# Optimization experiments

Measured on AMD Instinct MI355X. Metric: run time of the kernel, lower is better.

The kernel has to match this reference:

```python
import jax, jax.numpy as jnp
import numpy as np

EMB_DIM = 512
QKV_DIM = 512
NUM_HEADS = 8
HEAD_DIM = QKV_DIM // NUM_HEADS  # 64
BATCH = 4
SEQLEN = 2048


def _gaussian_orthogonal_random_matrix(rng, nb_rows, nb_cols):
    # Matches torch gaussian_orthogonal_random_matrix with scaling=0.
    blocks = []
    n_full = nb_rows // nb_cols
    for _ in range(n_full):
        q, _ = np.linalg.qr(rng.standard_normal((nb_cols, nb_cols)))
        blocks.append(q.T)
    rem = nb_rows - n_full * nb_cols
    if rem > 0:
        q, _ = np.linalg.qr(rng.standard_normal((nb_cols, nb_cols)))
        blocks.append(q.T[:rem])
    mat = np.concatenate(blocks, axis=0)
    mult = np.linalg.norm(rng.standard_normal((nb_rows, nb_cols)), axis=1)
    return (mult[:, None] * mat).astype(np.float32)


def setup_inputs() -> dict:
    key = jax.random.key(0)
    ks = jax.random.split(key, 9)
    s = 0.02
    inp = {
        'x': jax.random.normal(ks[0], (BATCH, SEQLEN, EMB_DIM), jnp.float32),
        'Wq': jax.random.normal(ks[1], (EMB_DIM, QKV_DIM), jnp.float32) * s,
        'bq': jnp.zeros((QKV_DIM,), jnp.float32),
        'Wk': jax.random.normal(ks[2], (EMB_DIM, QKV_DIM), jnp.float32) * s,
        'bk': jnp.zeros((QKV_DIM,), jnp.float32),
        'Wv': jax.random.normal(ks[3], (EMB_DIM, QKV_DIM), jnp.float32) * s,
        'bv': jnp.zeros((QKV_DIM,), jnp.float32),
        'Wo': jax.random.normal(ks[4], (QKV_DIM, EMB_DIM), jnp.float32) * s,
        'bo': jnp.zeros((EMB_DIM,), jnp.float32),
        'proj': jnp.asarray(_gaussian_orthogonal_random_matrix(
            np.random.default_rng(0), QKV_DIM, HEAD_DIM)),  # (m=qkv_dim, head_dim)
    }
    return inp


def _split_heads(x):
    b, s, _ = x.shape
    return x.reshape(b, s, NUM_HEADS, HEAD_DIM).transpose(0, 2, 1, 3)  # (b,h,s,d)


def _softmax_kernel(data, proj, is_query, eps=1e-4):
    # data: (b,h,n,d); proj: (m,d)
    d = data.shape[-1]
    dn = d ** -0.25                       # data normalizer
    ratio = proj.shape[0] ** -0.5         # m^{-1/2}
    data_dash = jnp.einsum('bhnd,md->bhnm', dn * data, proj)
    diag = jnp.sum(data * data, axis=-1, keepdims=True) * (0.5 * dn * dn)
    if is_query:
        m = jax.lax.stop_gradient(jnp.max(data_dash, axis=-1, keepdims=True))
    else:
        m = jax.lax.stop_gradient(jnp.max(data_dash, axis=(-1, -2), keepdims=True))
    return ratio * (jnp.exp(data_dash - diag - m) + eps)


def _linear_attn(q, k, v):
    # q,k: (b,h,n,m); v: (b,h,n,d)
    k_cumsum = jnp.sum(k, axis=-2)                                  # (b,h,m)
    d_inv = 1.0 / jnp.einsum('bhnm,bhm->bhn', q, k_cumsum)          # (b,h,n)
    context = jnp.einsum('bhnm,bhnd->bhmd', k, v)                   # (b,h,m,d)
    return jnp.einsum('bhmd,bhnm,bhn->bhnd', context, q, d_inv)


def reference(x, Wq, bq, Wk, bk, Wv, bv, Wo, bo, proj):
    q = _split_heads(x @ Wq + bq)
    k = _split_heads(x @ Wk + bk)
    v = _split_heads(x @ Wv + bv)
    qp = _softmax_kernel(q, proj, is_query=True)
    kp = _softmax_kernel(k, proj, is_query=False)
    out = _linear_attn(qp, kp, v)                                   # (b,h,n,d)
    b, h, n, d = out.shape
    out = out.transpose(0, 2, 1, 3).reshape(b, n, h * d)            # combine heads
    return out @ Wo + bo
```

## Files before the change

kernel.cpp:

```cpp
#include <hip/hip_runtime.h>

typedef unsigned short u16;
typedef unsigned int   u32;
typedef __attribute__((ext_vector_type(8))) short bf16x8;
typedef __attribute__((ext_vector_type(4))) short s16x4;
typedef __attribute__((ext_vector_type(4))) float f32x4;

#define MFMA16(a,b,c) __builtin_amdgcn_mfma_f32_16x16x32_bf16((a),(b),(c),0,0,0)

__device__ __forceinline__ float bf2f(u16 u){ return __uint_as_float(((u32)u)<<16); }
__device__ __forceinline__ u16 f2bf(float f){
  u32 u = __float_as_uint(f);
  return (u16)((u + 0x7fffu + ((u>>16)&1u)) >> 16);
}
__device__ __forceinline__ u32 encf(float f){ u32 u=__float_as_uint(f); return (u&0x80000000u)? ~u : (u|0x80000000u); }
__device__ __forceinline__ float decf(u32 u){ return (u&0x80000000u)? __uint_as_float(u&0x7fffffffu) : __uint_as_float(~u); }

__device__ __forceinline__ void async_lds16(u16* lds, const u16* g){
  __builtin_amdgcn_global_load_lds((const __attribute__((address_space(1))) void*)g,
                                   (__attribute__((address_space(3))) void*)lds,
                                   16, 0, 0);
}

template<int ROWS>
__device__ __forceinline__ void stage64(u16* dst, const u16* src, int srcStride, int tid){
  #pragma unroll
  for (int u=tid; u<ROWS*8; u+=256){
    int r=u>>3, c=(u&7)<<3;
    *(int4*)&dst[r*72+c] = *(const int4*)&src[(size_t)r*srcStride + c];
  }
}

__global__ void k_init(u32* kmaxEnc, u16* projS,
                       const float* __restrict__ proj, const float* __restrict__ x, u16* __restrict__ xb){
  int i = blockIdx.x*blockDim.x + threadIdx.x;
  int st = gridDim.x*blockDim.x;
  for (int j=i; j<32; j+=st) kmaxEnc[j]=0u;
  const float dn = 0.35355339059327373f;
  for (int j=i; j<512*64; j+=st) projS[j] = f2bf(dn*proj[j]);
  for (int j=i; j<524288; j+=st){
    float4 a = *(const float4*)&x[(size_t)j*8];
    float4 b = *(const float4*)&x[(size_t)j*8+4];
    u16 tmp[8] = {f2bf(a.x),f2bf(a.y),f2bf(a.z),f2bf(a.w),
                  f2bf(b.x),f2bf(b.y),f2bf(b.z),f2bf(b.w)};
    *(int4*)&xb[(size_t)j*8] = *(const int4*)tmp;
  }
}

__global__ __launch_bounds__(256) void k_trw(const float* s0, const float* s1, const float* s2, const float* s3,
                                             u16* d0, u16* d1, u16* d2, u16* d3){
  int z = blockIdx.z;
  const float* src = z==0?s0:(z==1?s1:(z==2?s2:s3));
  u16* dst         = z==0?d0:(z==1?d1:(z==2?d2:d3));
  __shared__ u16 t[32][34];
  int c0=blockIdx.x*32, r0=blockIdx.y*32;
  int tid=threadIdx.x;
  for (int u=tid; u<1024; u+=256){ int r=u>>5, c=u&31; t[r][c]=f2bf(src[(size_t)(r0+r)*512 + c0+c]); }
  __syncthreads();
  for (int u=tid; u<1024; u+=256){ int c=u>>5, r=u&31; dst[(size_t)(c0+c)*512 + r0+r]=t[r][c]; }
}

__global__ __launch_bounds__(256) void k_trv(const u16* __restrict__ v, u16* __restrict__ vT){
  int bh = blockIdx.z; int b=bh>>3, h=bh&7;
  int d0 = blockIdx.x*32, n0 = blockIdx.y*32;
  __shared__ u16 t[32][34];
  int tid=threadIdx.x;
  const u16* s = v + (size_t)(b*2048)*512 + h*64;
  for (int u=tid; u<1024; u+=256){ int r=u>>5, c=u&31; t[r][c]=s[(size_t)(n0+r)*512 + d0+c]; }
  __syncthreads();
  u16* d = vT + (size_t)bh*64*2048;
  for (int u=tid; u<1024; u+=256){ int c=u>>5, r=u&31; d[(size_t)(d0+c)*2048 + n0+r]=t[r][c]; }
}

__global__ __launch_bounds__(256) void k_vsum(const u16* __restrict__ vB, float* __restrict__ vsum){
  int bh=blockIdx.x; int b=bh>>3, h=bh&7;
  int tid=threadIdx.x; int d=tid&63, part=tid>>6;
  const u16* src = vB + (size_t)(b*2048 + part*512)*512 + h*64 + d;
  float s=0.f;
  for (int n=0;n<512;++n) s += bf2f(src[(size_t)n*512]);
  __shared__ float red[256];
  red[tid]=s; __syncthreads();
  if (part==0) vsum[bh*64+d]=red[d]+red[64+d]+red[128+d]+red[192+d];
}

__global__ __launch_bounds__(256) void k_kdiag(const u16* __restrict__ kB, float* __restrict__ diagK){
  int bh=blockIdx.x, seg=blockIdx.y;
  int b=bh>>3, h=bh&7;
  int tid=threadIdx.x;
  int part=tid&7;
  const u16* base = kB + (size_t)(b*2048 + seg*256)*512 + h*64 + part*8;
  for (int n0=0; n0<256; n0+=32){
    int n = n0 + (tid>>3);
    bf16x8 v = *(const bf16x8*)&base[(size_t)n*512];
    float sq=0.f;
    #pragma unroll
    for (int j=0;j<8;++j){ float f=bf2f((u16)v[j]); sq+=f*f; }
    sq += __shfl_xor(sq,1,64); sq += __shfl_xor(sq,2,64); sq += __shfl_xor(sq,4,64);
    if (part==0) diagK[(size_t)bh*2048 + seg*256 + n] = 0.0625f*sq;
  }
}

__global__ __launch_bounds__(256) void k_sums(const u16* __restrict__ ctxT, const float* __restrict__ kcs,
                                              float* __restrict__ ctxsum, float* __restrict__ kcssum){
  int bh = blockIdx.x;
  int tid = threadIdx.x;
  int d = tid&63, part = tid>>6;
  const u16* src = ctxT + (size_t)bh*64*512 + (size_t)d*512 + part*128;
  float s=0.f;
  for (int m=0;m<128;m+=8){
    bf16x8 v = *(const bf16x8*)&src[m];
    #pragma unroll
    for (int j=0;j<8;++j) s += bf2f((u16)v[j]);
  }
  __shared__ float red[256];
  __shared__ float red2[256];
  red[tid]=s;
  float t=0.f;
  for (int u=tid;u<512;u+=256) t += kcs[(size_t)bh*512+u];
  red2[tid]=t;
  __syncthreads();
  if (part==0) ctxsum[bh*64+d] = red[d]+red[64+d]+red[128+d]+red[192+d];
  if (tid<64){
    float a=red2[tid]+red2[tid+64]+red2[tid+128]+red2[tid+192];
    #pragma unroll
    for (int m2=1;m2<64;m2<<=1) a += __shfl_xor(a,m2,64);
    if (tid==0) kcssum[bh]=a;
  }
}

template<bool OF32>
__global__ __launch_bounds__(256) void k_gemm2(const u16* __restrict__ A,
    const u16* BT0, const u16* BT1, const u16* BT2,
    const float* b0, const float* b1, const float* b2,
    void* O0, void* O1, void* O2)
{
  int z = blockIdx.z;
  const u16* BT    = z==0?BT0:(z==1?BT1:BT2);
  const float* bias= z==0?b0 :(z==1?b1 :b2 );
  void* Ov         = z==0?O0 :(z==1?O1 :O2 );
  int bm = blockIdx.x*128, bn = blockIdx.y*64;
  __shared__ u16 sA[128*64];
  __shared__ u16 sB[64*64];
  int tid=threadIdx.x, w=tid>>6, lane=tid&63;
  int lr = lane>>3, lc = (lane&7)*8;
  f32x4 acc[8] = {};
  for (int kk=0; kk<512; kk+=64){
    __syncthreads();
    #pragma unroll
    for (int i=0;i<4;++i){
      int idx = w*4+i;
      async_lds16(&sA[idx*512], A + (size_t)(bm + idx*8 + lr)*512 + kk + lc);
    }
    #pragma unroll
    for (int i=0;i<2;++i){
      int idx = w*2+i;
      async_lds16(&sB[idx*512], BT + (size_t)(bn + idx*8 + lr)*512 + kk + lc);
    }
    __syncthreads();
    int fr = lane&15, kb=(lane>>4)*8;
    #pragma unroll
    for (int rt=0; rt<2; ++rt){
      int ar = (w*2+rt)*16 + fr;
      #pragma unroll
      for (int ct=0; ct<4; ++ct){
        int br = ct*16 + fr;
        #pragma unroll
        for (int kc=0; kc<2; ++kc){
          bf16x8 av = *(const bf16x8*)&sA[ar*64 + kc*32 + kb];
          bf16x8 bv = *(const bf16x8*)&sB[br*64 + kc*32 + kb];
          acc[rt*4+ct] = MFMA16(av,bv,acc[rt*4+ct]);
        }
      }
    }
  }
  int colg = lane&15, rowg=(lane>>4)*4;
  #pragma unroll
  for (int rt=0; rt<2; ++rt){
    #pragma unroll
    for (int ct=0; ct<4; ++ct){
      int col = bn + ct*16 + colg;
      float bv = bias[col];
      #pragma unroll
      for (int j=0;j<4;++j){
        int row = bm + (w*2+rt)*16 + rowg + j;
        if constexpr (OF32) ((float*)Ov)[(size_t)row*512 + col] = acc[rt*4+ct][j] + bv;
        else                ((u16*) Ov)[(size_t)row*512 + col] = f2bf(acc[rt*4+ct][j] + bv);
      }
    }
  }
}

__global__ __launch_bounds__(256) void k_kpctx3(const u16* __restrict__ kB, const u16* __restrict__ projS,
    const u16* __restrict__ vT, const float* __restrict__ diagK,
    float* __restrict__ ctxPT, float* __restrict__ kcsP, u32* __restrict__ kmaxEnc)
{
  int h=blockIdx.x, y=blockIdx.y, b=blockIdx.z;
  int mblk = y&7, s = y>>3;
  int bh=b*8+h;
  int m0 = mblk*64;
  __shared__ __align__(16) u16 sK[128*72];
  __shared__ __align__(16) u16 sV[64*136];
  __shared__ __align__(16) u16 sP[64*72];
  __shared__ __align__(16) u16 sT[64*136];
  __shared__ float sDg[128];
  __shared__ float red[4];
  int tid=threadIdx.x, w=tid>>6, lane=tid&63;
  int fr=lane&15, kb=(lane>>4)*8, rowg=(lane>>4)*4;
  stage64<64>(sP, projS + m0*64, 64, tid);
  f32x4 accc[4]={};
  float sS=0.f;
  float lm=-3.0e38f;
  const u16* gK = kB + (size_t)(b*2048 + s*1024)*512 + h*64;
  const u16* gV = vT + (size_t)bh*64*2048 + s*1024;
  const float* gD = diagK + (size_t)bh*2048 + s*1024;
  int4 pK[4], pV[4]; float4 pD={0.f,0.f,0.f,0.f};
  #pragma unroll
  for (int i=0;i<4;++i){ int u=tid+i*256; int r=u>>3,c=(u&7)<<3; pK[i]=*(const int4*)&gK[(size_t)r*512 + c]; }
  #pragma unroll
  for (int i=0;i<4;++i){ int u=tid+i*256; int r=u>>4,c=(u&15)<<3; pV[i]=*(const int4*)&gV[(size_t)r*2048 + c]; }
  if (tid<32) pD = *(const float4*)&gD[tid*4];
  for (int nc=0; nc<8; ++nc){
    #pragma unroll
    for (int i=0;i<4;++i){ int u=tid+i*256; int r=u>>3,c=(u&7)<<3; *(int4*)&sK[r*72+c]=pK[i]; }
    #pragma unroll
    for (int i=0;i<4;++i){ int u=tid+i*256; int r=u>>4,c=(u&15)<<3; *(int4*)&sV[r*136+c]=pV[i]; }
    if (tid<32) *(float4*)&sDg[tid*4] = pD;
    __syncthreads();
    if (nc<7){
      #pragma unroll
      for (int i=0;i<4;++i){ int u=tid+i*256; int r=u>>3,c=(u&7)<<3; pK[i]=*(const int4*)&gK[(size_t)((nc+1)*128+r)*512 + c]; }
      #pragma unroll
      for (int i=0;i<4;++i){ int u=tid+i*256; int r=u>>4,c=(u&15)<<3; pV[i]=*(const int4*)&gV[(size_t)r*2048 + (nc+1)*128 + c]; }
      if (tid<32) pD = *(const float4*)&gD[(nc+1)*128 + tid*4];
    }
    f32x4 facc[2][4];
    #pragma unroll
    for (int rt=0;rt<2;++rt){
      int ar=(w*2+rt)*16+fr;
      #pragma unroll
      for (int mt=0;mt<4;++mt){
        f32x4 a={0.f,0.f,0.f,0.f};
        a=MFMA16(*(const bf16x8*)&sK[ar*72+kb],    *(const bf16x8*)&sP[(mt*16+fr)*72+kb],    a);
        a=MFMA16(*(const bf16x8*)&sK[ar*72+32+kb], *(const bf16x8*)&sP[(mt*16+fr)*72+32+kb], a);
        facc[rt][mt]=a;
        lm=fmaxf(lm, fmaxf(fmaxf(a[0],a[1]),fmaxf(a[2],a[3])));
      }
    }
    #pragma unroll
    for (int rt=0;rt<2;++rt){
      int nl=(w*2+rt)*16+rowg;
      #pragma unroll
      for (int mt=0;mt<4;++mt){
        int ml=mt*16+fr;
        s16x4 pk;
        #pragma unroll
        for (int j=0;j<4;++j) pk[j]=(short)f2bf(__expf(facc[rt][mt][j]-sDg[nl+j]));
        *(s16x4*)&sT[ml*136+nl]=pk;
      }
    }
    __syncthreads();
    int am=w*16+fr;
    #pragma unroll
    for (int ct=0;ct<4;++ct){
      #pragma unroll
      for (int ks=0;ks<4;++ks){
        accc[ct]=MFMA16(*(const bf16x8*)&sT[am*136+ks*32+kb],
                        *(const bf16x8*)&sV[(ct*16+fr)*136+ks*32+kb], accc[ct]);
      }
    }
    {
      int m=tid>>2, q=tid&3;
      #pragma unroll
      for (int n8=0;n8<4;++n8){
        bf16x8 v=*(const bf16x8*)&sT[m*136+q*32+n8*8];
        #pragma unroll
        for (int j=0;j<8;++j) sS += bf2f((u16)v[j]);
      }
    }
    __syncthreads();
  }
  {
    int m=tid>>2, q=tid&3;
    float t=sS;
    t += __shfl_xor(t,1,64); t += __shfl_xor(t,2,64);
    if (q==0) kcsP[(size_t)(s*32+bh)*512 + m0 + m] = t;
  }
  #pragma unroll
  for (int m2=1;m2<64;m2<<=1) lm=fmaxf(lm,__shfl_xor(lm,m2,64));
  if (lane==0) red[w]=lm;
  __syncthreads();
  if (tid==0) atomicMax(&kmaxEnc[bh], encf(fmaxf(fmaxf(red[0],red[1]),fmaxf(red[2],red[3]))));
  float* sTf = (float*)sT;
  int mloc = w*16+rowg;
  #pragma unroll
  for (int ct=0;ct<4;++ct){
    #pragma unroll
    for (int j=0;j<4;++j) sTf[(ct*16+fr)*68 + mloc + j] = accc[ct][j];
  }
  __syncthreads();
  for (int u=tid; u<1024; u+=256){
    int r=u>>4, c=(u&15)*4;
    *(float4*)&ctxPT[((size_t)(s*32+bh)*64 + r)*512 + m0 + c] = *(const float4*)&sTf[r*68+c];
  }
}

__global__ __launch_bounds__(256) void k_comb(const float* __restrict__ ctxPT, u16* __restrict__ ctxT,
                                              const float* __restrict__ kcsP, float* __restrict__ kcs){
  int bh=blockIdx.x, dblk=blockIdx.y;
  int tid=threadIdx.x;
  int d0=dblk*8;
  const float* p0 = ctxPT + ((size_t)bh*64 + d0)*512;
  const float* p1 = ctxPT + ((size_t)(32+bh)*64 + d0)*512;
  u16* o = ctxT + ((size_t)bh*64 + d0)*512;
  for (int u=tid; u<1024; u+=256){
    int r=u>>7, c=(u&127)*4;
    float4 a=*(const float4*)&p0[(size_t)r*512+c];
    float4 bq=*(const float4*)&p1[(size_t)r*512+c];
    u16 t[4]={f2bf(a.x+bq.x),f2bf(a.y+bq.y),f2bf(a.z+bq.z),f2bf(a.w+bq.w)};
    *(int2*)&o[(size_t)r*512+c] = *(const int2*)t;
  }
  if (dblk==0){
    for (int u=tid; u<512; u+=256)
      kcs[(size_t)bh*512+u] = kcsP[(size_t)bh*512+u] + kcsP[(size_t)(32+bh)*512+u];
  }
}

__global__ __launch_bounds__(256) void k_qpout2(const u16* __restrict__ qB, const u16* __restrict__ projS,
    const float* __restrict__ kcs, const u16* __restrict__ ctxT,
    const float* __restrict__ ctxsum, const float* __restrict__ kcssum,
    const float* __restrict__ vsum, const u32* __restrict__ kmaxEnc,
    u16* __restrict__ outc)
{
  int h=blockIdx.x, chunk=blockIdx.y, b=blockIdx.z;
  int bh=b*8+h;
  int t0 = b*2048 + chunk*128;
  __shared__ u16 sP[2][64*64];
  __shared__ u16 sCt[2][64*64];
  __shared__ u16 qpL[128*72];
  __shared__ float sK[512];
  __shared__ float diag[128];
  int tid=threadIdx.x, w=tid>>6, lane=tid&63;
  int fr=lane&15, kb=(lane>>4)*8, rowg=(lane>>4)*4;
  bf16x8 qf[2][2];
  #pragma unroll
  for (int rt=0;rt<2;++rt)
    #pragma unroll
    for (int kc=0;kc<2;++kc)
      qf[rt][kc] = *(const bf16x8*)&qB[(size_t)(t0 + w*32 + rt*16 + fr)*512 + h*64 + kc*32 + kb];
  #pragma unroll
  for (int rt=0;rt<2;++rt){
    float s=0.f;
    #pragma unroll
    for (int kc=0;kc<2;++kc)
      #pragma unroll
      for (int j=0;j<8;++j){ float f=bf2f((u16)qf[rt][kc][j]); s+=f*f; }
    s += __shfl_xor(s,16,64); s += __shfl_xor(s,32,64);
    if (lane<16) diag[w*32 + rt*16 + fr] = 0.0625f*s;
  }
  for (int u=tid; u<512; u+=256) sK[u] = kcs[(size_t)bh*512 + u];
  {
    const u16* gp = projS;
    const u16* gc = ctxT + (size_t)bh*64*512;
    int lr=lane>>3, lc=(lane&7)*8;
    #pragma unroll
    for (int i=0;i<2;++i){
      int idx = w*2+i;
      async_lds16(&sP[0][idx*512], gp + idx*512 + lane*8);
      async_lds16(&sCt[0][idx*512], gc + (size_t)(idx*8+lr)*512 + lc);
    }
  }
  f32x4 acc2[2][4]={};
  float mx[2][4], dp[2][4], rs[2][4];
  #pragma unroll
  for (int rt=0;rt<2;++rt)
    #pragma unroll
    for (int j=0;j<4;++j){ mx[rt][j]=-3.0e38f; dp[rt][j]=0.f; rs[rt][j]=0.f; }
  __syncthreads();
  for (int mc=0; mc<8; ++mc){
    int cur = mc&1;
    if (mc<7){
      int nxt = cur^1;
      const u16* gp = projS + (mc+1)*64*64;
      const u16* gc = ctxT + (size_t)bh*64*512 + (mc+1)*64;
      int lr=lane>>3, lc=(lane&7)*8;
      #pragma unroll
      for (int i=0;i<2;++i){
        int idx = w*2+i;
        async_lds16(&sP[nxt][idx*512], gp + idx*512 + lane*8);
        async_lds16(&sCt[nxt][idx*512], gc + (size_t)(idx*8+lr)*512 + lc);
      }
    }
    f32x4 facc[2][4];
    #pragma unroll
    for (int rt=0;rt<2;++rt){
      #pragma unroll
      for (int mt=0;mt<4;++mt){
        f32x4 a={0.f,0.f,0.f,0.f};
        #pragma unroll
        for (int kc=0;kc<2;++kc){
          bf16x8 bv = *(const bf16x8*)&sP[cur][(mt*16+fr)*64 + kc*32 + kb];
          a = MFMA16(qf[rt][kc], bv, a);
        }
        facc[rt][mt]=a;
      }
    }
    #pragma unroll
    for (int rt=0;rt<2;++rt){
      #pragma unroll
      for (int mt=0;mt<4;++mt){
        #pragma unroll
        for (int j=0;j<4;++j){
          int rl = w*32 + rt*16 + rowg + j;
          mx[rt][j] = fmaxf(mx[rt][j], facc[rt][mt][j]);
          float vq = __expf(facc[rt][mt][j] - diag[rl]);
          u16 us = f2bf(vq);
          qpL[rl*72 + mt*16 + fr] = us;
          float uf = bf2f(us);
          dp[rt][j] += uf*sK[mc*64 + mt*16 + fr];
          rs[rt][j] += uf;
        }
      }
    }
    __syncthreads();
    #pragma unroll
    for (int rt=0;rt<2;++rt){
      #pragma unroll
      for (int ct=0;ct<4;++ct){
        #pragma unroll
        for (int kc=0;kc<2;++kc){
          bf16x8 av = *(const bf16x8*)&qpL[(w*32+rt*16+fr)*72 + kc*32 + kb];
          bf16x8 bv = *(const bf16x8*)&sCt[cur][(ct*16+fr)*64 + kc*32 + kb];
          acc2[rt][ct] = MFMA16(av,bv,acc2[rt][ct]);
        }
      }
    }
    __syncthreads();
  }
  #pragma unroll
  for (int rt=0;rt<2;++rt){
    #pragma unroll
    for (int j=0;j<4;++j){
      #pragma unroll
      for (int s=1;s<16;s<<=1){
        dp[rt][j] += __shfl_xor(dp[rt][j],s,64);
        rs[rt][j] += __shfl_xor(rs[rt][j],s,64);
        mx[rt][j]  = fmaxf(mx[rt][j], __shfl_xor(mx[rt][j],s,64));
      }
    }
  }
  float mk  = decf(kmaxEnc[bh]);
  float emk = __expf(mk);
  float Ssum = kcssum[bh];
  const float eps=1e-4f;
  float emq[2][4];
  #pragma unroll
  for (int rt=0;rt<2;++rt)
    #pragma unroll
    for (int j=0;j<4;++j) emq[rt][j]=__expf(mx[rt][j]);
  #pragma unroll
  for (int rt=0;rt<2;++rt){
    #pragma unroll
    for (int ct=0;ct<4;++ct){
      int d = ct*16 + fr;
      float cs = ctxsum[bh*64 + d];
      float vs = vsum[bh*64 + d];
      #pragma unroll
      for (int j=0;j<4;++j){
        float eq = emq[rt][j];
        float numer = acc2[rt][ct][j] + eps*(emk*vs*rs[rt][j] + eq*cs + eps*eq*emk*512.0f*vs);
        float den   = dp[rt][j]       + eps*(emk*2048.0f*rs[rt][j] + eq*Ssum + eps*eq*emk*512.0f*2048.0f);
        int row = t0 + w*32 + rt*16 + rowg + j;
        outc[(size_t)row*512 + h*64 + d] = f2bf(numer/den);
      }
    }
  }
}

extern "C" void kernel_launch(void* const* d_in, const int* in_sizes, int n_in,
                              void* d_out, int out_size, void* d_ws, size_t ws_size,
                              hipStream_t stream)
{
  (void)in_sizes; (void)n_in; (void)out_size; (void)ws_size;
  const float* x    = (const float*)d_in[0];
  const float* Wq   = (const float*)d_in[1];
  const float* bq   = (const float*)d_in[2];
  const float* Wk   = (const float*)d_in[3];
  const float* bk   = (const float*)d_in[4];
  const float* Wv   = (const float*)d_in[5];
  const float* bv   = (const float*)d_in[6];
  const float* Wo   = (const float*)d_in[7];
  const float* bo   = (const float*)d_in[8];
  const float* proj = (const float*)d_in[9];

  char* w = (char*)d_ws;
  size_t off=0;
  auto alloc=[&](size_t bytes)->char*{ char* p=w+off; off=(off+bytes+255)&~(size_t)255; return p; };
  u16*  xb   = (u16*)alloc(8192ull*512*2);
  u16*  qB   = (u16*)alloc(8192ull*512*2);
  u16*  kBf  = (u16*)alloc(8192ull*512*2);
  u16*  vB   = (u16*)alloc(8192ull*512*2);
  u16*  vT   = (u16*)alloc(32ull*64*2048*2);
  u16*  WqT  = (u16*)alloc(512ull*512*2);
  u16*  WkT  = (u16*)alloc(512ull*512*2);
  u16*  WvT  = (u16*)alloc(512ull*512*2);
  u16*  WoT  = (u16*)alloc(512ull*512*2);
  u16*  projS= (u16*)alloc(512ull*64*2);
  u16*  ctxT = (u16*)alloc(32ull*64*512*2);
  float* ctxPT=(float*)alloc(2ull*32*64*512*4);
  float* kcs = (float*)alloc(32ull*512*4);
  float* kcsP= (float*)alloc(2ull*32*512*4);
  float* diagK=(float*)alloc(32ull*2048*4);
  u32*  kmx  = (u32*)alloc(256);
  float* ctxs= (float*)alloc(32ull*64*4);
  float* kcss= (float*)alloc(32ull*4);
  float* vsm = (float*)alloc(32ull*64*4);
  u16*  outc = kBf;

  dim3 TB(256);
  k_init<<<dim3(256),TB,0,stream>>>(kmx,projS,proj,x,xb);
  k_trw<<<dim3(16,16,4),TB,0,stream>>>(Wq,Wk,Wv,Wo, WqT,WkT,WvT,WoT);
  k_gemm2<false><<<dim3(64,8,3),TB,0,stream>>>(xb, WqT,WkT,WvT, bq,bk,bv, qB,kBf,vB);
  k_trv<<<dim3(2,64,32),TB,0,stream>>>(vB, vT);
  k_vsum<<<dim3(32),TB,0,stream>>>(vB, vsm);
  k_kdiag<<<dim3(32,8),TB,0,stream>>>(kBf, diagK);
  k_kpctx3<<<dim3(8,16,4),TB,0,stream>>>(kBf, projS, vT, diagK, ctxPT, kcsP, kmx);
  k_comb<<<dim3(32,8),TB,0,stream>>>(ctxPT, ctxT, kcsP, kcs);
  k_sums<<<dim3(32),TB,0,stream>>>(ctxT, kcs, ctxs, kcss);
  k_qpout2<<<dim3(8,16,4),TB,0,stream>>>(qB, projS, kcs, ctxT, ctxs, kcss, vsm, kmx, outc);
  k_gemm2<true><<<dim3(64,8,1),TB,0,stream>>>(outc, WoT,WoT,WoT, bo,bo,bo,
                                              d_out,d_out,d_out);
}
```

Baseline: 157.3 us.

## Double-buffer GEMM LDS staging and use partial-vmcnt soft barriers

The QKV projection GEMM now double-buffers its A/B LDS tiles and prefetches the next K slice with async global-to-LDS loads while computing the current one. Barriers become explicit s_waitcnt with partial vmcnt counts plus s_barrier, so loads can stay in flight across the barrier. In the output kernel, ctxT gets a single buffer loaded each iteration, proj stays double-buffered, and waits use counted vmcnt. The aim is to overlap global load latency with MFMA work, at the cost of more LDS and fragile hand-counted vmcnt values that could cause races if miscounted.

```diff
diff --git a/kernel.cpp b/kernel.cpp
--- a/kernel.cpp
+++ b/kernel.cpp
@@ -7,6 +7,11 @@
 typedef __attribute__((ext_vector_type(4))) float f32x4;
 
 #define MFMA16(a,b,c) __builtin_amdgcn_mfma_f32_16x16x32_bf16((a),(b),(c),0,0,0)
+
+#define SOFT_BAR_LG() do{ asm volatile("s_waitcnt lgkmcnt(0)" ::: "memory"); \
+  __builtin_amdgcn_s_barrier(); __builtin_amdgcn_sched_barrier(0); }while(0)
+#define SOFT_BAR_VM(N) do{ asm volatile("s_waitcnt vmcnt(" #N ") lgkmcnt(0)" ::: "memory"); \
+  __builtin_amdgcn_s_barrier(); __builtin_amdgcn_sched_barrier(0); }while(0)
 
 __device__ __forceinline__ float bf2f(u16 u){ return __uint_as_float(((u32)u)<<16); }
 __device__ __forceinline__ u16 f2bf(float f){
@@ -139,25 +144,29 @@
   const float* bias= z==0?b0 :(z==1?b1 :b2 );
   void* Ov         = z==0?O0 :(z==1?O1 :O2 );
   int bm = blockIdx.x*128, bn = blockIdx.y*64;
-  __shared__ u16 sA[128*64];
-  __shared__ u16 sB[64*64];
+  __shared__ u16 sA[2][128*64];
+  __shared__ u16 sB[2][64*64];
   int tid=threadIdx.x, w=tid>>6, lane=tid&63;
   int lr = lane>>3, lc = (lane&7)*8;
   f32x4 acc[8] = {};
-  for (int kk=0; kk<512; kk+=64){
-    __syncthreads();
+  auto stage=[&](int bf, int koff){
     #pragma unroll
     for (int i=0;i<4;++i){
       int idx = w*4+i;
-      async_lds16(&sA[idx*512], A + (size_t)(bm + idx*8 + lr)*512 + kk + lc);
+      async_lds16(&sA[bf][idx*512], A + (size_t)(bm + idx*8 + lr)*512 + koff + lc);
     }
     #pragma unroll
     for (int i=0;i<2;++i){
       int idx = w*2+i;
-      async_lds16(&sB[idx*512], BT + (size_t)(bn + idx*8 + lr)*512 + kk + lc);
-    }
-    __syncthreads();
-    int fr = lane&15, kb=(lane>>4)*8;
+      async_lds16(&sB[bf][idx*512], BT + (size_t)(bn + idx*8 + lr)*512 + koff + lc);
+    }
+  };
+  stage(0, 0);
+  int fr = lane&15, kb=(lane>>4)*8;
+  for (int kk=0; kk<8; ++kk){
+    int cur = kk&1;
+    if (kk<7) stage(cur^1, (kk+1)*64);
+    if (kk<7) { SOFT_BAR_VM(6); } else { SOFT_BAR_VM(0); }
     #pragma unroll
     for (int rt=0; rt<2; ++rt){
       int ar = (w*2+rt)*16 + fr;
@@ -166,12 +175,13 @@
         int br = ct*16 + fr;
         #pragma unroll
         for (int kc=0; kc<2; ++kc){
-          bf16x8 av = *(const bf16x8*)&sA[ar*64 + kc*32 + kb];
-          bf16x8 bv = *(const bf16x8*)&sB[br*64 + kc*32 + kb];
+          bf16x8 av = *(const bf16x8*)&sA[cur][ar*64 + kc*32 + kb];
+          bf16x8 bv = *(const bf16x8*)&sB[cur][br*64 + kc*32 + kb];
           acc[rt*4+ct] = MFMA16(av,bv,acc[rt*4+ct]);
         }
       }
     }
+    SOFT_BAR_LG();
   }
   int colg = lane&15, rowg=(lane>>4)*4;
   #pragma unroll
@@ -225,7 +235,7 @@
     #pragma unroll
     for (int i=0;i<4;++i){ int u=tid+i*256; int r=u>>4,c=(u&15)<<3; *(int4*)&sV[r*136+c]=pV[i]; }
     if (tid<32) *(float4*)&sDg[tid*4] = pD;
-    __syncthreads();
+    SOFT_BAR_LG();
     if (nc<7){
       #pragma unroll
       for (int i=0;i<4;++i){ int u=tid+i*256; int r=u>>3,c=(u&7)<<3; pK[i]=*(const int4*)&gK[(size_t)((nc+1)*128+r)*512 + c]; }
@@ -258,7 +268,7 @@
         *(s16x4*)&sT[ml*136+nl]=pk;
       }
     }
-    __syncthreads();
+    SOFT_BAR_LG();
     int am=w*16+fr;
     #pragma unroll
     for (int ct=0;ct<4;++ct){
@@ -277,7 +287,7 @@
         for (int j=0;j<8;++j) sS += bf2f((u16)v[j]);
       }
     }
-    __syncthreads();
+    SOFT_BAR_LG();
   }
   {
     int m=tid>>2, q=tid&3;
@@ -335,12 +345,13 @@
   int bh=b*8+h;
   int t0 = b*2048 + chunk*128;
   __shared__ u16 sP[2][64*64];
-  __shared__ u16 sCt[2][64*64];
+  __shared__ u16 sCt[64*64];
   __shared__ u16 qpL[128*72];
   __shared__ float sK[512];
   __shared__ float diag[128];
   int tid=threadIdx.x, w=tid>>6, lane=tid&63;
   int fr=lane&15, kb=(lane>>4)*8, rowg=(lane>>4)*4;
+  int lr=lane>>3, lc=(lane&7)*8;
   bf16x8 qf[2][2];
   #pragma unroll
   for (int rt=0;rt<2;++rt)
@@ -358,36 +369,32 @@
     if (lane<16) diag[w*32 + rt*16 + fr] = 0.0625f*s;
   }
   for (int u=tid; u<512; u+=256) sK[u] = kcs[(size_t)bh*512 + u];
-  {
-    const u16* gp = projS;
-    const u16* gc = ctxT + (size_t)bh*64*512;
-    int lr=lane>>3, lc=(lane&7)*8;
+  const u16* gcB = ctxT + (size_t)bh*64*512;
+  #pragma unroll
+  for (int i=0;i<2;++i){
+    int idx = w*2+i;
+    async_lds16(&sP[0][idx*512], projS + idx*512 + lane*8);
+  }
+  f32x4 acc2[2][4]={};
+  float mx[2][4], dp[2][4], rs[2][4];
+  #pragma unroll
+  for (int rt=0;rt<2;++rt)
+    #pragma unroll
+    for (int j=0;j<4;++j){ mx[rt][j]=-3.0e38f; dp[rt][j]=0.f; rs[rt][j]=0.f; }
+  SOFT_BAR_VM(0);
+  for (int mc=0; mc<8; ++mc){
+    int cur = mc&1;
     #pragma unroll
     for (int i=0;i<2;++i){
       int idx = w*2+i;
-      async_lds16(&sP[0][idx*512], gp + idx*512 + lane*8);
-      async_lds16(&sCt[0][idx*512], gc + (size_t)(idx*8+lr)*512 + lc);
-    }
-  }
-  f32x4 acc2[2][4]={};
-  float mx[2][4], dp[2][4], rs[2][4];
-  #pragma unroll
-  for (int rt=0;rt<2;++rt)
-    #pragma unroll
-    for (int j=0;j<4;++j){ mx[rt][j]=-3.0e38f; dp[rt][j]=0.f; rs[rt][j]=0.f; }
-  __syncthreads();
-  for (int mc=0; mc<8; ++mc){
-    int cur = mc&1;
+      async_lds16(&sCt[idx*512], gcB + (size_t)(idx*8+lr)*512 + mc*64 + lc);
+    }
     if (mc<7){
-      int nxt = cur^1;
       const u16* gp = projS + (mc+1)*64*64;
-      const u16* gc = ctxT + (size_t)bh*64*512 + (mc+1)*64;
-      int lr=lane>>3, lc=(lane&7)*8;
       #pragma unroll
       for (int i=0;i<2;++i){
         int idx = w*2+i;
-        async_lds16(&sP[nxt][idx*512], gp + idx*512 + lane*8);
-        async_lds16(&sCt[nxt][idx*512], gc + (size_t)(idx*8+lr)*512 + lc);
+        async_lds16(&sP[cur^1][idx*512], gp + idx*512 + lane*8);
       }
     }
     f32x4 facc[2][4];
@@ -421,7 +428,7 @@
         }
       }
     }
-    __syncthreads();
+    if (mc<7) { SOFT_BAR_VM(2); } else { SOFT_BAR_VM(0); }
     #pragma unroll
     for (int rt=0;rt<2;++rt){
       #pragma unroll
@@ -429,12 +436,12 @@
         #pragma unroll
         for (int kc=0;kc<2;++kc){
           bf16x8 av = *(const bf16x8*)&qpL[(w*32+rt*16+fr)*72 + kc*32 + kb];
-          bf16x8 bv = *(const bf16x8*)&sCt[cur][(ct*16+fr)*64 + kc*32 + kb];
+          bf16x8 bv = *(const bf16x8*)&sCt[(ct*16+fr)*64 + kc*32 + kb];
           acc2[rt][ct] = MFMA16(av,bv,acc2[rt][ct]);
         }
       }
     }
-    __syncthreads();
+    if (mc<7) { SOFT_BAR_VM(0); }
   }
   #pragma unroll
   for (int rt=0;rt<2;++rt){
```

Measured after the change: 163.6 us. 4.0% more time.

## Merge setup and prep kernels, fuse sums into combine, register-accumulate kcs

Applied to the files above, without the earlier changes.

Folds k_init and k_trw into one k_setup launch, and k_trv, k_vsum and k_kdiag into one k_prep launch, using block-index ranges to pick the work. k_sums goes away: its ctx row sums and kcs totals are now computed inside k_comb2, the row sums via LDS atomics. In k_kpctx3 the key-feature column sums are kept in registers from the bf16-rounded exp values instead of re-reading sT from LDS, and one barrier is removed. The aim is fewer kernel launches and less redundant LDS traffic, at the cost of shared-memory atomics and heterogeneous blocks within a grid.

```diff
diff --git a/kernel.cpp b/kernel.cpp
--- a/kernel.cpp
+++ b/kernel.cpp
@@ -31,100 +31,75 @@
   }
 }
 
-__global__ void k_init(u32* kmaxEnc, u16* projS,
-                       const float* __restrict__ proj, const float* __restrict__ x, u16* __restrict__ xb){
-  int i = blockIdx.x*blockDim.x + threadIdx.x;
-  int st = gridDim.x*blockDim.x;
-  for (int j=i; j<32; j+=st) kmaxEnc[j]=0u;
-  const float dn = 0.35355339059327373f;
-  for (int j=i; j<512*64; j+=st) projS[j] = f2bf(dn*proj[j]);
-  for (int j=i; j<524288; j+=st){
-    float4 a = *(const float4*)&x[(size_t)j*8];
-    float4 b = *(const float4*)&x[(size_t)j*8+4];
-    u16 tmp[8] = {f2bf(a.x),f2bf(a.y),f2bf(a.z),f2bf(a.w),
-                  f2bf(b.x),f2bf(b.y),f2bf(b.z),f2bf(b.w)};
-    *(int4*)&xb[(size_t)j*8] = *(const int4*)tmp;
-  }
-}
-
-__global__ __launch_bounds__(256) void k_trw(const float* s0, const float* s1, const float* s2, const float* s3,
-                                             u16* d0, u16* d1, u16* d2, u16* d3){
-  int z = blockIdx.z;
-  const float* src = z==0?s0:(z==1?s1:(z==2?s2:s3));
-  u16* dst         = z==0?d0:(z==1?d1:(z==2?d2:d3));
-  __shared__ u16 t[32][34];
-  int c0=blockIdx.x*32, r0=blockIdx.y*32;
-  int tid=threadIdx.x;
-  for (int u=tid; u<1024; u+=256){ int r=u>>5, c=u&31; t[r][c]=f2bf(src[(size_t)(r0+r)*512 + c0+c]); }
-  __syncthreads();
-  for (int u=tid; u<1024; u+=256){ int c=u>>5, r=u&31; dst[(size_t)(c0+c)*512 + r0+r]=t[r][c]; }
-}
-
-__global__ __launch_bounds__(256) void k_trv(const u16* __restrict__ v, u16* __restrict__ vT){
-  int bh = blockIdx.z; int b=bh>>3, h=bh&7;
-  int d0 = blockIdx.x*32, n0 = blockIdx.y*32;
-  __shared__ u16 t[32][34];
-  int tid=threadIdx.x;
-  const u16* s = v + (size_t)(b*2048)*512 + h*64;
-  for (int u=tid; u<1024; u+=256){ int r=u>>5, c=u&31; t[r][c]=s[(size_t)(n0+r)*512 + d0+c]; }
-  __syncthreads();
-  u16* d = vT + (size_t)bh*64*2048;
-  for (int u=tid; u<1024; u+=256){ int c=u>>5, r=u&31; d[(size_t)(d0+c)*2048 + n0+r]=t[r][c]; }
-}
-
-__global__ __launch_bounds__(256) void k_vsum(const u16* __restrict__ vB, float* __restrict__ vsum){
-  int bh=blockIdx.x; int b=bh>>3, h=bh&7;
-  int tid=threadIdx.x; int d=tid&63, part=tid>>6;
-  const u16* src = vB + (size_t)(b*2048 + part*512)*512 + h*64 + d;
-  float s=0.f;
-  for (int n=0;n<512;++n) s += bf2f(src[(size_t)n*512]);
-  __shared__ float red[256];
-  red[tid]=s; __syncthreads();
-  if (part==0) vsum[bh*64+d]=red[d]+red[64+d]+red[128+d]+red[192+d];
-}
-
-__global__ __launch_bounds__(256) void k_kdiag(const u16* __restrict__ kB, float* __restrict__ diagK){
-  int bh=blockIdx.x, seg=blockIdx.y;
-  int b=bh>>3, h=bh&7;
-  int tid=threadIdx.x;
-  int part=tid&7;
-  const u16* base = kB + (size_t)(b*2048 + seg*256)*512 + h*64 + part*8;
-  for (int n0=0; n0<256; n0+=32){
-    int n = n0 + (tid>>3);
-    bf16x8 v = *(const bf16x8*)&base[(size_t)n*512];
-    float sq=0.f;
-    #pragma unroll
-    for (int j=0;j<8;++j){ float f=bf2f((u16)v[j]); sq+=f*f; }
-    sq += __shfl_xor(sq,1,64); sq += __shfl_xor(sq,2,64); sq += __shfl_xor(sq,4,64);
-    if (part==0) diagK[(size_t)bh*2048 + seg*256 + n] = 0.0625f*sq;
-  }
-}
-
-__global__ __launch_bounds__(256) void k_sums(const u16* __restrict__ ctxT, const float* __restrict__ kcs,
-                                              float* __restrict__ ctxsum, float* __restrict__ kcssum){
-  int bh = blockIdx.x;
-  int tid = threadIdx.x;
-  int d = tid&63, part = tid>>6;
-  const u16* src = ctxT + (size_t)bh*64*512 + (size_t)d*512 + part*128;
-  float s=0.f;
-  for (int m=0;m<128;m+=8){
-    bf16x8 v = *(const bf16x8*)&src[m];
-    #pragma unroll
-    for (int j=0;j<8;++j) s += bf2f((u16)v[j]);
-  }
-  __shared__ float red[256];
-  __shared__ float red2[256];
-  red[tid]=s;
-  float t=0.f;
-  for (int u=tid;u<512;u+=256) t += kcs[(size_t)bh*512+u];
-  red2[tid]=t;
-  __syncthreads();
-  if (part==0) ctxsum[bh*64+d] = red[d]+red[64+d]+red[128+d]+red[192+d];
-  if (tid<64){
-    float a=red2[tid]+red2[tid+64]+red2[tid+128]+red2[tid+192];
-    #pragma unroll
-    for (int m2=1;m2<64;m2<<=1) a += __shfl_xor(a,m2,64);
-    if (tid==0) kcssum[bh]=a;
+__global__ __launch_bounds__(256) void k_setup(u32* kmaxEnc, u16* projS,
+    const float* __restrict__ proj, const float* __restrict__ x, u16* __restrict__ xb,
+    const float* s0, const float* s1, const float* s2, const float* s3,
+    u16* d0, u16* d1, u16* d2, u16* d3)
+{
+  int bid=blockIdx.x, tid=threadIdx.x;
+  if (bid < 1024){
+    int z = bid>>8, t = bid&255;
+    const float* src = z==0?s0:(z==1?s1:(z==2?s2:s3));
+    u16* dst         = z==0?d0:(z==1?d1:(z==2?d2:d3));
+    __shared__ u16 tl[32][34];
+    int c0=(t&15)*32, r0=(t>>4)*32;
+    for (int u=tid; u<1024; u+=256){ int r=u>>5, c=u&31; tl[r][c]=f2bf(src[(size_t)(r0+r)*512 + c0+c]); }
+    __syncthreads();
+    for (int u=tid; u<1024; u+=256){ int c=u>>5, r=u&31; dst[(size_t)(c0+c)*512 + r0+r]=tl[r][c]; }
+  } else {
+    int i = (bid-1024)*256 + tid;
+    int st = 256*256;
+    for (int j=i; j<32; j+=st) kmaxEnc[j]=0u;
+    const float dn = 0.35355339059327373f;
+    for (int j=i; j<512*64; j+=st) projS[j] = f2bf(dn*proj[j]);
+    for (int j=i; j<524288; j+=st){
+      float4 a = *(const float4*)&x[(size_t)j*8];
+      float4 b = *(const float4*)&x[(size_t)j*8+4];
+      u16 tmp[8] = {f2bf(a.x),f2bf(a.y),f2bf(a.z),f2bf(a.w),
+                    f2bf(b.x),f2bf(b.y),f2bf(b.z),f2bf(b.w)};
+      *(int4*)&xb[(size_t)j*8] = *(const int4*)tmp;
+    }
+  }
+}
+
+__global__ __launch_bounds__(256) void k_prep(const u16* __restrict__ vB, u16* __restrict__ vT,
+    float* __restrict__ vsum, const u16* __restrict__ kB, float* __restrict__ diagK)
+{
+  int bid=blockIdx.x, tid=threadIdx.x;
+  if (bid < 4096){
+    int xx=bid&1, y=(bid>>1)&63, bh=bid>>7;
+    int b=bh>>3, h=bh&7;
+    int dd0=xx*32, n0=y*32;
+    __shared__ u16 t[32][34];
+    const u16* s = vB + (size_t)(b*2048)*512 + h*64;
+    for (int u=tid; u<1024; u+=256){ int r=u>>5, c=u&31; t[r][c]=s[(size_t)(n0+r)*512 + dd0+c]; }
+    __syncthreads();
+    u16* d = vT + (size_t)bh*64*2048;
+    for (int u=tid; u<1024; u+=256){ int c=u>>5, r=u&31; d[(size_t)(dd0+c)*2048 + n0+r]=t[r][c]; }
+  } else if (bid < 4128){
+    int bh=bid-4096; int b=bh>>3, h=bh&7;
+    int d=tid&63, part=tid>>6;
+    const u16* src = vB + (size_t)(b*2048 + part*512)*512 + h*64 + d;
+    float s=0.f;
+    for (int n=0;n<512;++n) s += bf2f(src[(size_t)n*512]);
+    __shared__ float red[256];
+    red[tid]=s; __syncthreads();
+    if (part==0) vsum[bh*64+d]=red[d]+red[64+d]+red[128+d]+red[192+d];
+  } else {
+    int idx=bid-4128;
+    int bh=idx&31, seg=idx>>5;
+    int b=bh>>3, h=bh&7;
+    int part=tid&7;
+    const u16* base = kB + (size_t)(b*2048 + seg*256)*512 + h*64 + part*8;
+    for (int n0=0; n0<256; n0+=32){
+      int n = n0 + (tid>>3);
+      bf16x8 v = *(const bf16x8*)&base[(size_t)n*512];
+      float sq=0.f;
+      #pragma unroll
+      for (int j=0;j<8;++j){ float f=bf2f((u16)v[j]); sq+=f*f; }
+      sq += __shfl_xor(sq,1,64); sq += __shfl_xor(sq,2,64); sq += __shfl_xor(sq,4,64);
+      if (part==0) diagK[(size_t)bh*2048 + seg*256 + n] = 0.0625f*sq;
+    }
   }
 }
 
@@ -204,11 +179,12 @@
   __shared__ __align__(16) u16 sT[64*136];
   __shared__ float sDg[128];
   __shared__ float red[4];
+  __shared__ float sRed[4][64];
   int tid=threadIdx.x, w=tid>>6, lane=tid&63;
-  int fr=lane&15, kb=(lane>>4)*8, rowg=(lane>>4)*4;
+  int fr=lane&15, kbg=lane>>4, kb=kbg*8, rowg=kbg*4;
   stage64<64>(sP, projS + m0*64, 64, tid);
   f32x4 accc[4]={};
-  float sS=0.f;
+  float sSm[4]={0.f,0.f,0.f,0.f};
   float lm=-3.0e38f;
   const u16* gK = kB + (size_t)(b*2048 + s*1024)*512 + h*64;
   const u16* gV = vT + (size_t)bh*64*2048 + s*1024;
@@ -254,7 +230,12 @@
         int ml=mt*16+fr;
         s16x4 pk;
         #pragma unroll
-        for (int j=0;j<4;++j) pk[j]=(short)f2bf(__expf(facc[rt][mt][j]-sDg[nl+j]));
+        for (int j=0;j<4;++j){
+          float vk = __expf(facc[rt][mt][j]-sDg[nl+j]);
+          u16 us = f2bf(vk);
+          pk[j]=(short)us;
+          sSm[mt] += bf2f(us);
+        }
         *(s16x4*)&sT[ml*136+nl]=pk;
       }
     }
@@ -268,47 +249,45 @@
                         *(const bf16x8*)&sV[(ct*16+fr)*136+ks*32+kb], accc[ct]);
       }
     }
-    {
-      int m=tid>>2, q=tid&3;
-      #pragma unroll
-      for (int n8=0;n8<4;++n8){
-        bf16x8 v=*(const bf16x8*)&sT[m*136+q*32+n8*8];
-        #pragma unroll
-        for (int j=0;j<8;++j) sS += bf2f((u16)v[j]);
-      }
-    }
-    __syncthreads();
-  }
-  {
-    int m=tid>>2, q=tid&3;
-    float t=sS;
-    t += __shfl_xor(t,1,64); t += __shfl_xor(t,2,64);
-    if (q==0) kcsP[(size_t)(s*32+bh)*512 + m0 + m] = t;
+    __syncthreads();
+  }
+  #pragma unroll
+  for (int mt=0;mt<4;++mt){
+    float t=sSm[mt];
+    t += __shfl_xor(t,16,64); t += __shfl_xor(t,32,64);
+    if (kbg==0) sRed[w][mt*16+fr]=t;
   }
   #pragma unroll
   for (int m2=1;m2<64;m2<<=1) lm=fmaxf(lm,__shfl_xor(lm,m2,64));
   if (lane==0) red[w]=lm;
+  float* sTf = (float*)sT;
+  int mloc = w*16+rowg;
+  #pragma unroll
+  for (int ct=0;ct<4;++ct){
+    #pragma unroll
+    for (int j=0;j<4;++j) sTf[(ct*16+fr)*68 + mloc + j] = accc[ct][j];
+  }
   __syncthreads();
   if (tid==0) atomicMax(&kmaxEnc[bh], encf(fmaxf(fmaxf(red[0],red[1]),fmaxf(red[2],red[3]))));
-  float* sTf = (float*)sT;
-  int mloc = w*16+rowg;
-  #pragma unroll
-  for (int ct=0;ct<4;++ct){
-    #pragma unroll
-    for (int j=0;j<4;++j) sTf[(ct*16+fr)*68 + mloc + j] = accc[ct][j];
-  }
-  __syncthreads();
+  if (tid<64) kcsP[(size_t)(s*32+bh)*512 + m0 + tid] =
+      sRed[0][tid]+sRed[1][tid]+sRed[2][tid]+sRed[3][tid];
   for (int u=tid; u<1024; u+=256){
     int r=u>>4, c=(u&15)*4;
     *(float4*)&ctxPT[((size_t)(s*32+bh)*64 + r)*512 + m0 + c] = *(const float4*)&sTf[r*68+c];
   }
 }
 
-__global__ __launch_bounds__(256) void k_comb(const float* __restrict__ ctxPT, u16* __restrict__ ctxT,
-                                              const float* __restrict__ kcsP, float* __restrict__ kcs){
+__global__ __launch_bounds__(256) void k_comb2(const float* __restrict__ ctxPT, u16* __restrict__ ctxT,
+    const float* __restrict__ kcsP, float* __restrict__ kcs,
+    float* __restrict__ ctxsum, float* __restrict__ kcssum)
+{
   int bh=blockIdx.x, dblk=blockIdx.y;
   int tid=threadIdx.x;
   int d0=dblk*8;
+  __shared__ float sDsum[8];
+  __shared__ float sKsum[256];
+  if (tid<8) sDsum[tid]=0.f;
+  __syncthreads();
   const float* p0 = ctxPT + ((size_t)bh*64 + d0)*512;
   const float* p1 = ctxPT + ((size_t)(32+bh)*64 + d0)*512;
   u16* o = ctxT + ((size_t)bh*64 + d0)*512;
@@ -316,12 +295,27 @@
     int r=u>>7, c=(u&127)*4;
     float4 a=*(const float4*)&p0[(size_t)r*512+c];
     float4 bq=*(const float4*)&p1[(size_t)r*512+c];
-    u16 t[4]={f2bf(a.x+bq.x),f2bf(a.y+bq.y),f2bf(a.z+bq.z),f2bf(a.w+bq.w)};
+    float vx=a.x+bq.x, vy=a.y+bq.y, vz=a.z+bq.z, vw=a.w+bq.w;
+    u16 t[4]={f2bf(vx),f2bf(vy),f2bf(vz),f2bf(vw)};
     *(int2*)&o[(size_t)r*512+c] = *(const int2*)t;
-  }
+    atomicAdd(&sDsum[r], bf2f(t[0])+bf2f(t[1])+bf2f(t[2])+bf2f(t[3]));
+  }
+  float tpart=0.f;
   if (dblk==0){
-    for (int u=tid; u<512; u+=256)
-      kcs[(size_t)bh*512+u] = kcsP[(size_t)bh*512+u] + kcsP[(size_t)(32+bh)*512+u];
+    for (int u=tid; u<512; u+=256){
+      float t = kcsP[(size_t)bh*512+u] + kcsP[(size_t)(32+bh)*512+u];
+      kcs[(size_t)bh*512+u]=t;
+      tpart += t;
+    }
+  }
+  sKsum[tid]=tpart;
+  __syncthreads();
+  if (tid<8) ctxsum[bh*64 + d0 + tid] = sDsum[tid];
+  if (dblk==0 && tid<64){
+    float a=sKsum[tid]+sKsum[tid+64]+sKsum[tid+128]+sKsum[tid+192];
+    #pragma unroll
+    for (int m2=1;m2<64;m2<<=1) a += __shfl_xor(a,m2,64);
+    if (tid==0) kcssum[bh]=a;
   }
 }
 
@@ -517,15 +511,11 @@
   u16*  outc = kBf;
 
   dim3 TB(256);
-  k_init<<<dim3(256),TB,0,stream>>>(kmx,projS,proj,x,xb);
-  k_trw<<<dim3(16,16,4),TB,0,stream>>>(Wq,Wk,Wv,Wo, WqT,WkT,WvT,WoT);
+  k_setup<<<dim3(1280),TB,0,stream>>>(kmx,projS,proj,x,xb, Wq,Wk,Wv,Wo, WqT,WkT,WvT,WoT);
   k_gemm2<false><<<dim3(64,8,3),TB,0,stream>>>(xb, WqT,WkT,WvT, bq,bk,bv, qB,kBf,vB);
-  k_trv<<<dim3(2,64,32),TB,0,stream>>>(vB, vT);
-  k_vsum<<<dim3(32),TB,0,stream>>>(vB, vsm);
-  k_kdiag<<<dim3(32,8),TB,0,stream>>>(kBf, diagK);
+  k_prep<<<dim3(4384),TB,0,stream>>>(vB, vT, vsm, kBf, diagK);
   k_kpctx3<<<dim3(8,16,4),TB,0,stream>>>(kBf, projS, vT, diagK, ctxPT, kcsP, kmx);
-  k_comb<<<dim3(32,8),TB,0,stream>>>(ctxPT, ctxT, kcsP, kcs);
-  k_sums<<<dim3(32),TB,0,stream>>>(ctxT, kcs, ctxs, kcss);
+  k_comb2<<<dim3(32,8),TB,0,stream>>>(ctxPT, ctxT, kcsP, kcs, ctxs, kcss);
   k_qpout2<<<dim3(8,16,4),TB,0,stream>>>(qB, projS, kcs, ctxT, ctxs, kcss, vsm, kmx, outc);
   k_gemm2<true><<<dim3(64,8,1),TB,0,stream>>>(outc, WoT,WoT,WoT, bo,bo,bo,
                                               d_out,d_out,d_out);
```

New measurement: 147.2 us (median of 2 runs). -6.4%, faster.
